# Performance work log

Measured on AMD Instinct MI355X. Metric: run time of the kernel, lower is better.

## Reference

```python
import jax, jax.numpy as jnp
import numpy as np

N_NODES = 10000
N_EDGES = 80000
F_NODE = 16
F_EDGE = 8
BN_EPS = 1e-5


def _nnconv(x, src, dst, edge_attr, w1, b1, w2, b2, w_root, bias, cin, cout):
    # edge MLP -> per-edge weight matrices [E, cin, cout]
    h = jax.nn.relu(edge_attr @ w1 + b1) @ w2 + b2
    w = h.reshape(-1, cin, cout)
    # gather source node features, per-edge matmul
    msg = jnp.einsum('ei,eio->eo', x[src], w)  # [E, cout]
    # scatter-mean into target nodes
    deg = jax.ops.segment_sum(jnp.ones(msg.shape[0], x.dtype), dst, num_segments=N_NODES)
    agg = jax.ops.segment_sum(msg, dst, num_segments=N_NODES) / jnp.clip(deg, 1.0)[:, None]
    return x @ w_root + agg + bias


def _batchnorm(x, gamma, beta):
    m = jnp.mean(x, axis=0)
    v = jnp.mean((x - m) ** 2, axis=0)  # biased var, as torch BN training mode
    return (x - m) * jax.lax.rsqrt(v + BN_EPS) * gamma + beta


def setup_inputs() -> dict:
    key = jax.random.key(0)
    ks = jax.random.split(key, 24)
    s = 0.05
    inp = {
        'x': jax.random.normal(ks[0], (N_NODES, F_NODE), jnp.float32),
        'edge_index': jax.random.randint(ks[1], (2, N_EDGES), 0, N_NODES, jnp.int32),
        'edge_attr': jax.random.normal(ks[2], (N_EDGES, F_EDGE), jnp.float32),
        # conv1 edge MLP: F_EDGE -> 25 -> 32*F_NODE
        'nn1_w1': jax.random.normal(ks[3], (F_EDGE, 25), jnp.float32) * s,
        'nn1_b1': jnp.zeros((25,), jnp.float32),
        'nn1_w2': jax.random.normal(ks[4], (25, 32 * F_NODE), jnp.float32) * s,
        'nn1_b2': jnp.zeros((32 * F_NODE,), jnp.float32),
        'conv1_root': jax.random.normal(ks[5], (F_NODE, 32), jnp.float32) * s,
        'conv1_bias': jnp.zeros((32,), jnp.float32),
        'bn1_gamma': jnp.ones((32,), jnp.float32),
        'bn1_beta': jnp.zeros((32,), jnp.float32),
        # conv2 edge MLP: F_EDGE -> 25 -> 32*64
        'nn2_w1': jax.random.normal(ks[6], (F_EDGE, 25), jnp.float32) * s,
        'nn2_b1': jnp.zeros((25,), jnp.float32),
        'nn2_w2': jax.random.normal(ks[7], (25, 32 * 64), jnp.float32) * s,
        'nn2_b2': jnp.zeros((32 * 64,), jnp.float32),
        'conv2_root': jax.random.normal(ks[8], (32, 64), jnp.float32) * s,
        'conv2_bias': jnp.zeros((64,), jnp.float32),
        'bn2_gamma': jnp.ones((64,), jnp.float32),
        'bn2_beta': jnp.zeros((64,), jnp.float32),
        'fc1_w': jax.random.normal(ks[9], (64, 128), jnp.float32) * s,
        'fc1_b': jnp.zeros((128,), jnp.float32),
        'fc2_w': jax.random.normal(ks[10], (128, 1), jnp.float32) * s,
        'fc2_b': jnp.zeros((1,), jnp.float32),
    }
    return inp


def reference(x, edge_index, edge_attr,
              nn1_w1, nn1_b1, nn1_w2, nn1_b2, conv1_root, conv1_bias, bn1_gamma, bn1_beta,
              nn2_w1, nn2_b1, nn2_w2, nn2_b2, conv2_root, conv2_bias, bn2_gamma, bn2_beta,
              fc1_w, fc1_b, fc2_w, fc2_b):
    src, dst = edge_index[0], edge_index[1]
    h = jax.nn.elu(_nnconv(x, src, dst, edge_attr, nn1_w1, nn1_b1, nn1_w2, nn1_b2,
                           conv1_root, conv1_bias, F_NODE, 32))
    h = jax.nn.elu(_batchnorm(h, bn1_gamma, bn1_beta))
    h = jax.nn.elu(_nnconv(h, src, dst, edge_attr, nn2_w1, nn2_b1, nn2_w2, nn2_b2,
                           conv2_root, conv2_bias, 32, 64))
    h = jax.nn.elu(_batchnorm(h, bn2_gamma, bn2_beta))
    h = jax.nn.elu(h @ fc1_w + fc1_b)
    h = jax.nn.elu(h @ fc2_w + fc2_b)  # [N, 1]
    # single graph: sum over all nodes -> shape [1]
    return jnp.sum(h).reshape(1)
```

## Files before the change

### kernel.cpp

```cpp
#include <hip/hip_runtime.h>
#include <hip/hip_fp16.h>

#define N_NODES 10000
#define N_EDGES 80000
#define FN 16
#define FE 8
#define HID 25
#define C1 32
#define C2 64
#define HROW 28
#define SLOTS 40
#define SC_BLOCKS ((N_EDGES + 255) / 256)
#define NU_BLOCKS 512
#define FC_BLOCKS 640
#define TB1 16
#define TB2 8
#define M1 ((HID + 1) * C1)
#define M2 ((HID + 1) * C2)

typedef _Float16 h16;
typedef _Float16 h16x4 __attribute__((ext_vector_type(4)));

__device__ __forceinline__ float elu_f(float x) { return x > 0.f ? x : (expf(x) - 1.f); }

__device__ __forceinline__ float hdot(const h16* __restrict__ row, const float* Pk) {
    const h16x4* rv = (const h16x4*)row;
    float sx = 0.f, sy = 0.f, sz = 0.f, sw = 0.f;
#pragma unroll
    for (int q = 0; q < 7; q++) {
        h16x4 hv = rv[q];
        sx += (float)hv.x * Pk[4 * q];
        sy += (float)hv.y * Pk[4 * q + 1];
        sz += (float)hv.z * Pk[4 * q + 2];
        sw += (float)hv.w * Pk[4 * q + 3];
    }
    return (sx + sy) + (sz + sw);
}

__device__ __forceinline__ void msg1_edges(const float* Pk, int beg, int end,
                                           const int* __restrict__ ebuf,
                                           const h16* __restrict__ h1r,
                                           float* __restrict__ agg, int lane, int o) {
    int idx = beg;
    for (; idx + 3 < end; idx += 4) {
        int p0 = ebuf[idx], p1 = ebuf[idx + 1], p2 = ebuf[idx + 2], p3 = ebuf[idx + 3];
        float s0 = hdot(h1r + (size_t)(p0 >> 14) * HROW, Pk);
        float s1 = hdot(h1r + (size_t)(p1 >> 14) * HROW, Pk);
        float s2 = hdot(h1r + (size_t)(p2 >> 14) * HROW, Pk);
        float s3 = hdot(h1r + (size_t)(p3 >> 14) * HROW, Pk);
        float va = (lane < 32) ? s0 : s1;
        int da = (lane < 32) ? (p0 & 0x3FFF) : (p1 & 0x3FFF);
        atomicAdd(&agg[da * C1 + o], va);
        float vb = (lane < 32) ? s2 : s3;
        int db = (lane < 32) ? (p2 & 0x3FFF) : (p3 & 0x3FFF);
        atomicAdd(&agg[db * C1 + o], vb);
    }
    for (; idx + 1 < end; idx += 2) {
        int p0 = ebuf[idx], p1 = ebuf[idx + 1];
        float s0 = hdot(h1r + (size_t)(p0 >> 14) * HROW, Pk);
        float s1 = hdot(h1r + (size_t)(p1 >> 14) * HROW, Pk);
        float va = (lane < 32) ? s0 : s1;
        int da = (lane < 32) ? (p0 & 0x3FFF) : (p1 & 0x3FFF);
        atomicAdd(&agg[da * C1 + o], va);
    }
    if (idx < end) {
        int p0 = ebuf[idx];
        float s0 = hdot(h1r + (size_t)(p0 >> 14) * HROW, Pk);
        if (lane < 32) atomicAdd(&agg[(p0 & 0x3FFF) * C1 + o], s0);
    }
}

__device__ __forceinline__ void msg2_edges(const float* Pk, int beg, int end,
                                           const int* __restrict__ ebuf,
                                           const h16* __restrict__ h2r,
                                           float* __restrict__ agg, int lane) {
    int idx = beg;
    for (; idx + 3 < end; idx += 4) {
        int p0 = ebuf[idx], p1 = ebuf[idx + 1], p2 = ebuf[idx + 2], p3 = ebuf[idx + 3];
        float s0 = hdot(h2r + (size_t)(p0 >> 14) * HROW, Pk);
        float s1 = hdot(h2r + (size_t)(p1 >> 14) * HROW, Pk);
        float s2 = hdot(h2r + (size_t)(p2 >> 14) * HROW, Pk);
        float s3 = hdot(h2r + (size_t)(p3 >> 14) * HROW, Pk);
        atomicAdd(&agg[(p0 & 0x3FFF) * C2 + lane], s0);
        atomicAdd(&agg[(p1 & 0x3FFF) * C2 + lane], s1);
        atomicAdd(&agg[(p2 & 0x3FFF) * C2 + lane], s2);
        atomicAdd(&agg[(p3 & 0x3FFF) * C2 + lane], s3);
    }
    for (; idx < end; idx++) {
        int p0 = ebuf[idx];
        float s0 = hdot(h2r + (size_t)(p0 >> 14) * HROW, Pk);
        atomicAdd(&agg[(p0 & 0x3FFF) * C2 + lane], s0);
    }
}

__global__ void k_scatter(const float* __restrict__ ea, const int* __restrict__ ei,
                          const float* __restrict__ w1a, const float* __restrict__ b1a,
                          const float* __restrict__ w1b, const float* __restrict__ b1b,
                          int* __restrict__ cnt_src, int* __restrict__ cnt_dst,
                          int* __restrict__ ebuf, h16* __restrict__ h1r,
                          h16* __restrict__ h2r) {
    int tid = threadIdx.x;
    __shared__ float sw1a[FE * HID], sw1b[FE * HID], sb1a[HID], sb1b[HID];
    for (int i = tid; i < FE * HID; i += 256) { sw1a[i] = w1a[i]; sw1b[i] = w1b[i]; }
    if (tid < HID) { sb1a[tid] = b1a[tid]; sb1b[tid] = b1b[tid]; }
    __syncthreads();
    int e = blockIdx.x * 256 + tid;
    if (e >= N_EDGES) return;
    float a[FE];
#pragma unroll
    for (int i = 0; i < FE; i++) a[i] = ea[e * FE + i];
    int src = ei[e], dst = ei[N_EDGES + e];
    int slot = atomicAdd(&cnt_src[src], 1);
    if (slot < SLOTS) ebuf[src * SLOTS + slot] = (e << 14) | dst;
    atomicAdd(&cnt_dst[dst], 1);
    h16 b1buf[HROW], b2buf[HROW];
#pragma unroll
    for (int k = 0; k < HID; k++) {
        float s1 = sb1a[k], s2 = sb1b[k];
#pragma unroll
        for (int i = 0; i < FE; i++) { s1 += a[i] * sw1a[i * HID + k]; s2 += a[i] * sw1b[i * HID + k]; }
        b1buf[k] = (h16)fmaxf(s1, 0.f);
        b2buf[k] = (h16)fmaxf(s2, 0.f);
    }
    b1buf[25] = (h16)1.f; b1buf[26] = (h16)0.f; b1buf[27] = (h16)0.f;
    b2buf[25] = (h16)1.f; b2buf[26] = (h16)0.f; b2buf[27] = (h16)0.f;
    h16x4* h1p = (h16x4*)(h1r + (size_t)e * HROW);
    h16x4* h2p = (h16x4*)(h2r + (size_t)e * HROW);
#pragma unroll
    for (int q = 0; q < 7; q++) {
        h1p[q] = ((const h16x4*)b1buf)[q];
        h2p[q] = ((const h16x4*)b2buf)[q];
    }
}

__global__ __launch_bounds__(256, 4)
void k_conv1(const float* __restrict__ x, const float* __restrict__ w2,
             const float* __restrict__ b2, const int* __restrict__ cnt_src,
             const int* __restrict__ ebuf, const h16* __restrict__ h1r,
             float* __restrict__ agg) {
    __shared__ h16 Pl[TB1 * M1];
    __shared__ float xs[TB1 * FN];
    int tid = threadIdx.x;
    int n0 = blockIdx.x * TB1;
    for (int t = tid; t < TB1 * FN; t += 256) xs[t] = x[(size_t)n0 * FN + t];
    __syncthreads();
#pragma unroll
    for (int mm = 0; mm < 4; mm++) {
        int m = mm * 256 + tid;
        if (m < M1) {
            int k = m >> 5, o = m & 31;
            float wreg[FN];
            if (k < HID) {
#pragma unroll
                for (int i = 0; i < FN; i++) wreg[i] = w2[(size_t)(k * FN + i) * C1 + o];
            } else {
#pragma unroll
                for (int i = 0; i < FN; i++) wreg[i] = b2[i * C1 + o];
            }
#pragma unroll 2
            for (int n = 0; n < TB1; n++) {
                float s0 = 0.f, s1 = 0.f, s2 = 0.f, s3 = 0.f;
#pragma unroll
                for (int i = 0; i < FN; i += 4) {
                    s0 += xs[n * FN + i]     * wreg[i];
                    s1 += xs[n * FN + i + 1] * wreg[i + 1];
                    s2 += xs[n * FN + i + 2] * wreg[i + 2];
                    s3 += xs[n * FN + i + 3] * wreg[i + 3];
                }
                Pl[n * M1 + m] = (h16)((s0 + s1) + (s2 + s3));
            }
        }
    }
    __syncthreads();
    int lane = tid & 63, wv = tid >> 6, o = lane & 31;
    for (int dn = wv; dn < TB1; dn += 4) {
        int n = n0 + dn;
        float Pk[HROW];
#pragma unroll
        for (int k = 0; k <= HID; k++) Pk[k] = (float)Pl[dn * M1 + k * C1 + o];
        Pk[26] = 0.f; Pk[27] = 0.f;
        int deg = cnt_src[n];
        deg = deg < SLOTS ? deg : SLOTS;
        msg1_edges(Pk, n * SLOTS, n * SLOTS + deg, ebuf, h1r, agg, lane, o);
    }
}

template <int CIN, int COUT>
__global__ void k_node_update(const float* __restrict__ xin, const float* __restrict__ root,
                              const float* __restrict__ bias, const float* __restrict__ agg,
                              const int* __restrict__ degi, float* __restrict__ act,
                              float* __restrict__ s1g, float* __restrict__ s2g,
                              float* zero_out) {
    __shared__ float l1[256], l2[256];
    int tid = threadIdx.x;
    if (zero_out && blockIdx.x == 0 && tid == 0) *zero_out = 0.f;
    int o = tid % COUT;
    float b = bias[o];
    float rcol[CIN];
#pragma unroll
    for (int i = 0; i < CIN; i++) rcol[i] = root[i * COUT + o];
    float acc1 = 0.f, acc2 = 0.f;
    for (int t = blockIdx.x * 256 + tid; t < N_NODES * COUT; t += NU_BLOCKS * 256) {
        int n = t / COUT;
        const float* xr = xin + (size_t)n * CIN;
        float s0 = b, s1 = 0.f, s2 = 0.f, s3 = 0.f;
#pragma unroll
        for (int i = 0; i < CIN; i += 4) {
            s0 += xr[i]     * rcol[i];
            s1 += xr[i + 1] * rcol[i + 1];
            s2 += xr[i + 2] * rcol[i + 2];
            s3 += xr[i + 3] * rcol[i + 3];
        }
        float s = (s0 + s1) + (s2 + s3);
        s += agg[t] / fmaxf((float)degi[n], 1.0f);
        float a = elu_f(s);
        act[t] = a;
        acc1 += a; acc2 += a * a;
    }
    l1[tid] = acc1; l2[tid] = acc2;
    __syncthreads();
    for (int s = 128; s >= COUT; s >>= 1) {
        if (tid < s) { l1[tid] += l1[tid + s]; l2[tid] += l2[tid + s]; }
        __syncthreads();
    }
    if (tid < COUT) { atomicAdd(&s1g[tid], l1[tid]); atomicAdd(&s2g[tid], l2[tid]); }
}

__global__ __launch_bounds__(256, 4)
void k_conv2(const float* __restrict__ a1, const float* __restrict__ s1g,
             const float* __restrict__ s2g, const float* __restrict__ gamma,
             const float* __restrict__ beta, const float* __restrict__ w2,
             const float* __restrict__ b2, const int* __restrict__ cnt_src,
             const int* __restrict__ ebuf, const h16* __restrict__ h2r,
             float* __restrict__ agg, float* __restrict__ h1v) {
    __shared__ h16 Pl[TB2 * M2];
    __shared__ float xs[TB2 * C1];
    int tid = threadIdx.x;
    int n0 = blockIdx.x * TB2;
    for (int t = tid; t < TB2 * C1; t += 256) {
        int o = t & 31;
        float m = s1g[o] * (1.0f / N_NODES);
        float v = s2g[o] * (1.0f / N_NODES) - m * m;
        float sc = rsqrtf(v + 1e-5f) * gamma[o];
        float sh = beta[o] - m * sc;
        float val = elu_f(a1[(size_t)n0 * C1 + t] * sc + sh);
        xs[t] = val;
        h1v[(size_t)n0 * C1 + t] = val;
    }
    __syncthreads();
#pragma unroll
    for (int mm = 0; mm < 7; mm++) {
        int m = mm * 256 + tid;
        if (m < M2) {
            int k = m >> 6, o = m & 63;
            float wreg[C1];
            if (k < HID) {
#pragma unroll
                for (int i = 0; i < C1; i++) wreg[i] = w2[(size_t)(k * C1 + i) * C2 + o];
            } else {
#pragma unroll
                for (int i = 0; i < C1; i++) wreg[i] = b2[i * C2 + o];
            }
#pragma unroll 2
            for (int n = 0; n < TB2; n++) {
                float s0 = 0.f, s1 = 0.f, s2 = 0.f, s3 = 0.f;
#pragma unroll
                for (int i = 0; i < C1; i += 4) {
                    s0 += xs[n * C1 + i]     * wreg[i];
                    s1 += xs[n * C1 + i + 1] * wreg[i + 1];
                    s2 += xs[n * C1 + i + 2] * wreg[i + 2];
                    s3 += xs[n * C1 + i + 3] * wreg[i + 3];
                }
                Pl[n * M2 + m] = (h16)((s0 + s1) + (s2 + s3));
            }
        }
    }
    __syncthreads();
    int lane = tid & 63, wv = tid >> 6;
    for (int dn = wv; dn < TB2; dn += 4) {
        int n = n0 + dn;
        float Pk[HROW];
#pragma unroll
        for (int k = 0; k <= HID; k++) Pk[k] = (float)Pl[dn * M2 + k * C2 + lane];
        Pk[26] = 0.f; Pk[27] = 0.f;
        int deg = cnt_src[n];
        deg = deg < SLOTS ? deg : SLOTS;
        msg2_edges(Pk, n * SLOTS, n * SLOTS + deg, ebuf, h2r, agg, lane);
    }
}

__global__ void k_fc_sum(const float* __restrict__ a2,
                         const float* __restrict__ s1g, const float* __restrict__ s2g,
                         const float* __restrict__ gamma, const float* __restrict__ beta,
                         const float* __restrict__ fc1w, const float* __restrict__ fc1b,
                         const float* __restrict__ fc2w, const float* __restrict__ fc2b,
                         float* __restrict__ out) {
    int tid = threadIdx.x;
    int lane = tid & 63;
    int wave = tid >> 6;
    float m = s1g[lane] * (1.0f / N_NODES);
    float var = s2g[lane] * (1.0f / N_NODES) - m * m;
    float scale = rsqrtf(var + 1e-5f) * gamma[lane];
    float shift = beta[lane] - m * scale;
    float b0 = fc1b[lane], b1 = fc1b[lane + 64];
    float w0 = fc2w[lane], w1 = fc2w[lane + 64];
    float fb = fc2b[0];
    float acc = 0.f;
    for (int n = blockIdx.x * 4 + wave; n < N_NODES; n += FC_BLOCKS * 4) {
        float hval = elu_f(a2[(size_t)n * C2 + lane] * scale + shift);
        float s0 = b0, s1 = b1;
#pragma unroll
        for (int i = 0; i < C2; i++) {
            float hv = __shfl(hval, i);
            s0 += hv * fc1w[i * 128 + lane];
            s1 += hv * fc1w[i * 128 + 64 + lane];
        }
        float v = elu_f(s0) * w0 + elu_f(s1) * w1;
#pragma unroll
        for (int off2 = 32; off2 > 0; off2 >>= 1) v += __shfl_down(v, off2);
        if (lane == 0) acc += elu_f(v + fb);
    }
    __shared__ float lds[4];
    if (lane == 0) lds[wave] = acc;
    __syncthreads();
    if (tid == 0) atomicAdd(out, lds[0] + lds[1] + lds[2] + lds[3]);
}

extern "C" void kernel_launch(void* const* d_in, const int* in_sizes, int n_in,
                              void* d_out, int out_size, void* d_ws, size_t ws_size,
                              hipStream_t stream) {
    const float* x       = (const float*)d_in[0];
    const int*   ei      = (const int*)d_in[1];
    const float* ea      = (const float*)d_in[2];
    const float* nn1_w1  = (const float*)d_in[3];
    const float* nn1_b1  = (const float*)d_in[4];
    const float* nn1_w2  = (const float*)d_in[5];
    const float* nn1_b2  = (const float*)d_in[6];
    const float* c1_root = (const float*)d_in[7];
    const float* c1_bias = (const float*)d_in[8];
    const float* bn1_g   = (const float*)d_in[9];
    const float* bn1_b   = (const float*)d_in[10];
    const float* nn2_w1  = (const float*)d_in[11];
    const float* nn2_b1  = (const float*)d_in[12];
    const float* nn2_w2  = (const float*)d_in[13];
    const float* nn2_b2  = (const float*)d_in[14];
    const float* c2_root = (const float*)d_in[15];
    const float* c2_bias = (const float*)d_in[16];
    const float* bn2_g   = (const float*)d_in[17];
    const float* bn2_b   = (const float*)d_in[18];
    const float* fc1_w   = (const float*)d_in[19];
    const float* fc1_b   = (const float*)d_in[20];
    const float* fc2_w   = (const float*)d_in[21];
    const float* fc2_b   = (const float*)d_in[22];
    float* out = (float*)d_out;

    char* ws = (char*)d_ws;
    size_t off = 0;
    auto alloc = [&](size_t nbytes) -> void* {
        void* q = (void*)(ws + off);
        off += nbytes;
        off = (off + 255) & ~(size_t)255;
        return q;
    };
    int*   cnt_src = (int*)alloc(N_NODES * 4);
    int*   cnt_dst = (int*)alloc(N_NODES * 4);
    float* agg1    = (float*)alloc((size_t)N_NODES * C1 * 4);
    float* agg2    = (float*)alloc((size_t)N_NODES * C2 * 4);
    float* bn1_s1  = (float*)alloc(C1 * 4);
    float* bn1_s2  = (float*)alloc(C1 * 4);
    float* bn2_s1  = (float*)alloc(C2 * 4);
    float* bn2_s2  = (float*)alloc(C2 * 4);
    size_t zero_bytes = off;
    int*   ebuf = (int*)alloc((size_t)N_NODES * SLOTS * 4);
    h16*   h1r  = (h16*)alloc((size_t)N_EDGES * HROW * 2);
    h16*   h2r  = (h16*)alloc((size_t)N_EDGES * HROW * 2);
    float* a1   = (float*)alloc((size_t)N_NODES * C1 * 4);
    float* h1v  = (float*)alloc((size_t)N_NODES * C1 * 4);
    float* a2   = (float*)alloc((size_t)N_NODES * C2 * 4);
    (void)ws_size; (void)in_sizes; (void)n_in; (void)out_size;

    hipMemsetAsync(d_ws, 0, zero_bytes, stream);

    k_scatter<<<SC_BLOCKS, 256, 0, stream>>>(ea, ei, nn1_w1, nn1_b1, nn2_w1, nn2_b1,
                                             cnt_src, cnt_dst, ebuf, h1r, h2r);
    k_conv1<<<N_NODES / TB1, 256, 0, stream>>>(x, nn1_w2, nn1_b2, cnt_src, ebuf, h1r, agg1);
    k_node_update<FN, C1><<<NU_BLOCKS, 256, 0, stream>>>(x, c1_root, c1_bias, agg1,
                                                         cnt_dst, a1, bn1_s1, bn1_s2, nullptr);
    k_conv2<<<N_NODES / TB2, 256, 0, stream>>>(a1, bn1_s1, bn1_s2, bn1_g, bn1_b,
                                               nn2_w2, nn2_b2, cnt_src, ebuf, h2r, agg2, h1v);
    k_node_update<C1, C2><<<NU_BLOCKS, 256, 0, stream>>>(h1v, c2_root, c2_bias, agg2,
                                                         cnt_dst, a2, bn2_s1, bn2_s2, out);
    k_fc_sum<<<FC_BLOCKS, 256, 0, stream>>>(a2, bn2_s1, bn2_s2, bn2_g, bn2_b,
                                            fc1_w, fc1_b, fc2_w, fc2_b, out);
}
```

Before: 254.5 us.

## Use packed fp16 dot products and precompute conv1 node projections in scatter kernel

```diff
diff --git a/kernel.cpp b/kernel.cpp
--- a/kernel.cpp
+++ b/kernel.cpp
@@ -13,41 +13,43 @@
 #define SC_BLOCKS ((N_EDGES + 255) / 256)
 #define NU_BLOCKS 512
 #define FC_BLOCKS 640
-#define TB1 16
+#define TN 25
 #define TB2 8
 #define M1 ((HID + 1) * C1)
 #define M2 ((HID + 1) * C2)
+#define PRE1_BLOCKS (((M1 + 255) / 256) * (N_NODES / TN))
 
 typedef _Float16 h16;
+typedef _Float16 h16x2 __attribute__((ext_vector_type(2)));
 typedef _Float16 h16x4 __attribute__((ext_vector_type(4)));
+typedef _Float16 h16x8 __attribute__((ext_vector_type(8)));
 
 __device__ __forceinline__ float elu_f(float x) { return x > 0.f ? x : (expf(x) - 1.f); }
 
-__device__ __forceinline__ float hdot(const h16* __restrict__ row, const float* Pk) {
-    const h16x4* rv = (const h16x4*)row;
-    float sx = 0.f, sy = 0.f, sz = 0.f, sw = 0.f;
-#pragma unroll
-    for (int q = 0; q < 7; q++) {
-        h16x4 hv = rv[q];
-        sx += (float)hv.x * Pk[4 * q];
-        sy += (float)hv.y * Pk[4 * q + 1];
-        sz += (float)hv.z * Pk[4 * q + 2];
-        sw += (float)hv.w * Pk[4 * q + 3];
-    }
-    return (sx + sy) + (sz + sw);
-}
-
-__device__ __forceinline__ void msg1_edges(const float* Pk, int beg, int end,
+__device__ __forceinline__ float hdot13(const h16* __restrict__ row, const h16x2* Pk2) {
+    const h16x2* rv = (const h16x2*)row;
+    h16x2 a0 = {(h16)0.f, (h16)0.f};
+    h16x2 a1 = a0;
+#pragma unroll
+    for (int q = 0; q < 12; q += 2) {
+        a0 += rv[q] * Pk2[q];
+        a1 += rv[q + 1] * Pk2[q + 1];
+    }
+    a0 += rv[12] * Pk2[12];
+    return (float)a0.x + (float)a0.y + (float)a1.x + (float)a1.y;
+}
+
+__device__ __forceinline__ void msg1_edges(const h16x2* Pk2, int beg, int end,
                                            const int* __restrict__ ebuf,
                                            const h16* __restrict__ h1r,
                                            float* __restrict__ agg, int lane, int o) {
     int idx = beg;
     for (; idx + 3 < end; idx += 4) {
         int p0 = ebuf[idx], p1 = ebuf[idx + 1], p2 = ebuf[idx + 2], p3 = ebuf[idx + 3];
-        float s0 = hdot(h1r + (size_t)(p0 >> 14) * HROW, Pk);
-        float s1 = hdot(h1r + (size_t)(p1 >> 14) * HROW, Pk);
-        float s2 = hdot(h1r + (size_t)(p2 >> 14) * HROW, Pk);
-        float s3 = hdot(h1r + (size_t)(p3 >> 14) * HROW, Pk);
+        float s0 = hdot13(h1r + (size_t)(p0 >> 14) * HROW, Pk2);
+        float s1 = hdot13(h1r + (size_t)(p1 >> 14) * HROW, Pk2);
+        float s2 = hdot13(h1r + (size_t)(p2 >> 14) * HROW, Pk2);
+        float s3 = hdot13(h1r + (size_t)(p3 >> 14) * HROW, Pk2);
         float va = (lane < 32) ? s0 : s1;
         int da = (lane < 32) ? (p0 & 0x3FFF) : (p1 & 0x3FFF);
         atomicAdd(&agg[da * C1 + o], va);
@@ -57,30 +59,30 @@
     }
     for (; idx + 1 < end; idx += 2) {
         int p0 = ebuf[idx], p1 = ebuf[idx + 1];
-        float s0 = hdot(h1r + (size_t)(p0 >> 14) * HROW, Pk);
-        float s1 = hdot(h1r + (size_t)(p1 >> 14) * HROW, Pk);
+        float s0 = hdot13(h1r + (size_t)(p0 >> 14) * HROW, Pk2);
+        float s1 = hdot13(h1r + (size_t)(p1 >> 14) * HROW, Pk2);
         float va = (lane < 32) ? s0 : s1;
         int da = (lane < 32) ? (p0 & 0x3FFF) : (p1 & 0x3FFF);
         atomicAdd(&agg[da * C1 + o], va);
     }
     if (idx < end) {
         int p0 = ebuf[idx];
-        float s0 = hdot(h1r + (size_t)(p0 >> 14) * HROW, Pk);
+        float s0 = hdot13(h1r + (size_t)(p0 >> 14) * HROW, Pk2);
         if (lane < 32) atomicAdd(&agg[(p0 & 0x3FFF) * C1 + o], s0);
     }
 }
 
-__device__ __forceinline__ void msg2_edges(const float* Pk, int beg, int end,
+__device__ __forceinline__ void msg2_edges(const h16x2* Pk2, int beg, int end,
                                            const int* __restrict__ ebuf,
                                            const h16* __restrict__ h2r,
                                            float* __restrict__ agg, int lane) {
     int idx = beg;
     for (; idx + 3 < end; idx += 4) {
         int p0 = ebuf[idx], p1 = ebuf[idx + 1], p2 = ebuf[idx + 2], p3 = ebuf[idx + 3];
-        float s0 = hdot(h2r + (size_t)(p0 >> 14) * HROW, Pk);
-        float s1 = hdot(h2r + (size_t)(p1 >> 14) * HROW, Pk);
-        float s2 = hdot(h2r + (size_t)(p2 >> 14) * HROW, Pk);
-        float s3 = hdot(h2r + (size_t)(p3 >> 14) * HROW, Pk);
+        float s0 = hdot13(h2r + (size_t)(p0 >> 14) * HROW, Pk2);
+        float s1 = hdot13(h2r + (size_t)(p1 >> 14) * HROW, Pk2);
+        float s2 = hdot13(h2r + (size_t)(p2 >> 14) * HROW, Pk2);
+        float s3 = hdot13(h2r + (size_t)(p3 >> 14) * HROW, Pk2);
         atomicAdd(&agg[(p0 & 0x3FFF) * C2 + lane], s0);
         atomicAdd(&agg[(p1 & 0x3FFF) * C2 + lane], s1);
         atomicAdd(&agg[(p2 & 0x3FFF) * C2 + lane], s2);
@@ -88,23 +90,63 @@
     }
     for (; idx < end; idx++) {
         int p0 = ebuf[idx];
-        float s0 = hdot(h2r + (size_t)(p0 >> 14) * HROW, Pk);
+        float s0 = hdot13(h2r + (size_t)(p0 >> 14) * HROW, Pk2);
         atomicAdd(&agg[(p0 & 0x3FFF) * C2 + lane], s0);
     }
 }
 
-__global__ void k_scatter(const float* __restrict__ ea, const int* __restrict__ ei,
-                          const float* __restrict__ w1a, const float* __restrict__ b1a,
-                          const float* __restrict__ w1b, const float* __restrict__ b1b,
-                          int* __restrict__ cnt_src, int* __restrict__ cnt_dst,
-                          int* __restrict__ ebuf, h16* __restrict__ h1r,
-                          h16* __restrict__ h2r) {
+__device__ __forceinline__ void pre1_unit(const float* __restrict__ xin,
+                                          const float* __restrict__ w2,
+                                          const float* __restrict__ b2,
+                                          h16* __restrict__ P, int u, int tid) {
+    constexpr int MB = (M1 + 255) / 256;
+    int mb = u % MB;
+    int n0 = (u / MB) * TN;
+    int m = mb * 256 + tid;
+    if (m >= M1) return;
+    int k = m >> 5, o = m & 31;
+    float wreg[FN];
+    if (k < HID) {
+#pragma unroll
+        for (int i = 0; i < FN; i++) wreg[i] = w2[(size_t)(k * FN + i) * C1 + o];
+    } else {
+#pragma unroll
+        for (int i = 0; i < FN; i++) wreg[i] = b2[i * C1 + o];
+    }
+    int pmo = (k >> 1) * (2 * C1) + o * 2 + (k & 1);
+    for (int n = n0; n < n0 + TN; n++) {
+        const float* xr = xin + (size_t)n * FN;
+        float s0 = 0.f, s1 = 0.f, s2 = 0.f, s3 = 0.f;
+#pragma unroll
+        for (int i = 0; i < FN; i += 4) {
+            s0 += xr[i] * wreg[i];
+            s1 += xr[i + 1] * wreg[i + 1];
+            s2 += xr[i + 2] * wreg[i + 2];
+            s3 += xr[i + 3] * wreg[i + 3];
+        }
+        P[(size_t)n * M1 + pmo] = (h16)((s0 + s1) + (s2 + s3));
+    }
+}
+
+__global__ void k_scatter_pre1(const float* __restrict__ ea, const int* __restrict__ ei,
+                               const float* __restrict__ w1a, const float* __restrict__ b1a,
+                               const float* __restrict__ w1b, const float* __restrict__ b1b,
+                               const float* __restrict__ x, const float* __restrict__ w2a,
+                               const float* __restrict__ b2a,
+                               int* __restrict__ cnt_src, int* __restrict__ cnt_dst,
+                               int* __restrict__ ebuf, h16* __restrict__ h1r,
+                               h16* __restrict__ h2r, h16* __restrict__ P1) {
     int tid = threadIdx.x;
+    int bid = blockIdx.x;
+    if (bid >= SC_BLOCKS) {
+        pre1_unit(x, w2a, b2a, P1, bid - SC_BLOCKS, tid);
+        return;
+    }
     __shared__ float sw1a[FE * HID], sw1b[FE * HID], sb1a[HID], sb1b[HID];
     for (int i = tid; i < FE * HID; i += 256) { sw1a[i] = w1a[i]; sw1b[i] = w1b[i]; }
     if (tid < HID) { sb1a[tid] = b1a[tid]; sb1b[tid] = b1b[tid]; }
     __syncthreads();
-    int e = blockIdx.x * 256 + tid;
+    int e = bid * 256 + tid;
     if (e >= N_EDGES) return;
     float a[FE];
 #pragma unroll
@@ -133,56 +175,20 @@
     }
 }
 
-__global__ __launch_bounds__(256, 4)
-void k_conv1(const float* __restrict__ x, const float* __restrict__ w2,
-             const float* __restrict__ b2, const int* __restrict__ cnt_src,
-             const int* __restrict__ ebuf, const h16* __restrict__ h1r,
-             float* __restrict__ agg) {
-    __shared__ h16 Pl[TB1 * M1];
-    __shared__ float xs[TB1 * FN];
-    int tid = threadIdx.x;
-    int n0 = blockIdx.x * TB1;
-    for (int t = tid; t < TB1 * FN; t += 256) xs[t] = x[(size_t)n0 * FN + t];
-    __syncthreads();
-#pragma unroll
-    for (int mm = 0; mm < 4; mm++) {
-        int m = mm * 256 + tid;
-        if (m < M1) {
-            int k = m >> 5, o = m & 31;
-            float wreg[FN];
-            if (k < HID) {
-#pragma unroll
-                for (int i = 0; i < FN; i++) wreg[i] = w2[(size_t)(k * FN + i) * C1 + o];
-            } else {
-#pragma unroll
-                for (int i = 0; i < FN; i++) wreg[i] = b2[i * C1 + o];
-            }
-#pragma unroll 2
-            for (int n = 0; n < TB1; n++) {
-                float s0 = 0.f, s1 = 0.f, s2 = 0.f, s3 = 0.f;
-#pragma unroll
-                for (int i = 0; i < FN; i += 4) {
-                    s0 += xs[n * FN + i]     * wreg[i];
-                    s1 += xs[n * FN + i + 1] * wreg[i + 1];
-                    s2 += xs[n * FN + i + 2] * wreg[i + 2];
-                    s3 += xs[n * FN + i + 3] * wreg[i + 3];
-                }
-                Pl[n * M1 + m] = (h16)((s0 + s1) + (s2 + s3));
-            }
-        }
-    }
-    __syncthreads();
-    int lane = tid & 63, wv = tid >> 6, o = lane & 31;
-    for (int dn = wv; dn < TB1; dn += 4) {
-        int n = n0 + dn;
-        float Pk[HROW];
-#pragma unroll
-        for (int k = 0; k <= HID; k++) Pk[k] = (float)Pl[dn * M1 + k * C1 + o];
-        Pk[26] = 0.f; Pk[27] = 0.f;
-        int deg = cnt_src[n];
-        deg = deg < SLOTS ? deg : SLOTS;
-        msg1_edges(Pk, n * SLOTS, n * SLOTS + deg, ebuf, h1r, agg, lane, o);
-    }
+__global__ void k_conv1(const h16x2* __restrict__ P1p, const int* __restrict__ cnt_src,
+                        const int* __restrict__ ebuf, const h16* __restrict__ h1r,
+                        float* __restrict__ agg) {
+    int lane = threadIdx.x & 63;
+    int o = lane & 31;
+    int n = __builtin_amdgcn_readfirstlane(blockIdx.x * 4 + (threadIdx.x >> 6));
+    if (n >= N_NODES) return;
+    h16x2 Pk2[13];
+    const h16x2* Pr = P1p + (size_t)n * (M1 / 2) + o;
+#pragma unroll
+    for (int kk = 0; kk < 13; kk++) Pk2[kk] = Pr[kk * C1];
+    int deg = cnt_src[n];
+    deg = deg < SLOTS ? deg : SLOTS;
+    msg1_edges(Pk2, n * SLOTS, n * SLOTS + deg, ebuf, h1r, agg, lane, o);
 }
 
 template <int CIN, int COUT>
@@ -233,59 +239,70 @@
              const float* __restrict__ b2, const int* __restrict__ cnt_src,
              const int* __restrict__ ebuf, const h16* __restrict__ h2r,
              float* __restrict__ agg, float* __restrict__ h1v) {
-    __shared__ h16 Pl[TB2 * M2];
-    __shared__ float xs[TB2 * C1];
+    __shared__ h16 Pl_h[TB2 * M2];
+    __shared__ h16 xs_h[C1 * TB2];
     int tid = threadIdx.x;
     int n0 = blockIdx.x * TB2;
-    for (int t = tid; t < TB2 * C1; t += 256) {
-        int o = t & 31;
+    {
+        int n = tid >> 5, o = tid & 31;
         float m = s1g[o] * (1.0f / N_NODES);
         float v = s2g[o] * (1.0f / N_NODES) - m * m;
         float sc = rsqrtf(v + 1e-5f) * gamma[o];
         float sh = beta[o] - m * sc;
-        float val = elu_f(a1[(size_t)n0 * C1 + t] * sc + sh);
-        xs[t] = val;
-        h1v[(size_t)n0 * C1 + t] = val;
+        float val = elu_f(a1[(size_t)n0 * C1 + tid] * sc + sh);
+        xs_h[o * TB2 + n] = (h16)val;
+        h1v[(size_t)n0 * C1 + tid] = val;
     }
     __syncthreads();
+    const h16x8* xsv = (const h16x8*)xs_h;
 #pragma unroll
     for (int mm = 0; mm < 7; mm++) {
         int m = mm * 256 + tid;
         if (m < M2) {
             int k = m >> 6, o = m & 63;
-            float wreg[C1];
+            h16x2 wh[C1];
             if (k < HID) {
 #pragma unroll
-                for (int i = 0; i < C1; i++) wreg[i] = w2[(size_t)(k * C1 + i) * C2 + o];
+                for (int i = 0; i < C1; i++) {
+                    h16 w = (h16)w2[(size_t)(k * C1 + i) * C2 + o];
+                    wh[i] = (h16x2){w, w};
+                }
             } else {
 #pragma unroll
-                for (int i = 0; i < C1; i++) wreg[i] = b2[i * C2 + o];
+                for (int i = 0; i < C1; i++) {
+                    h16 w = (h16)b2[i * C2 + o];
+                    wh[i] = (h16x2){w, w};
+                }
             }
-#pragma unroll 2
-            for (int n = 0; n < TB2; n++) {
-                float s0 = 0.f, s1 = 0.f, s2 = 0.f, s3 = 0.f;
-#pragma unroll
-                for (int i = 0; i < C1; i += 4) {
-                    s0 += xs[n * C1 + i]     * wreg[i];
-                    s1 += xs[n * C1 + i + 1] * wreg[i + 1];
-                    s2 += xs[n * C1 + i + 2] * wreg[i + 2];
-                    s3 += xs[n * C1 + i + 3] * wreg[i + 3];
-                }
-                Pl[n * M2 + m] = (h16)((s0 + s1) + (s2 + s3));
+            h16x2 acc0 = {(h16)0.f, (h16)0.f};
+            h16x2 acc1 = acc0, acc2 = acc0, acc3 = acc0;
+#pragma unroll
+            for (int i = 0; i < C1; i++) {
+                h16x8 xv = xsv[i];
+                acc0 += __builtin_shufflevector(xv, xv, 0, 1) * wh[i];
+                acc1 += __builtin_shufflevector(xv, xv, 2, 3) * wh[i];
+                acc2 += __builtin_shufflevector(xv, xv, 4, 5) * wh[i];
+                acc3 += __builtin_shufflevector(xv, xv, 6, 7) * wh[i];
             }
+            int pmo = (k >> 1) * (2 * C2) + o * 2 + (k & 1);
+            h16* Plr = Pl_h + pmo;
+            Plr[0 * M2] = acc0.x; Plr[1 * M2] = acc0.y;
+            Plr[2 * M2] = acc1.x; Plr[3 * M2] = acc1.y;
+            Plr[4 * M2] = acc2.x; Plr[5 * M2] = acc2.y;
+            Plr[6 * M2] = acc3.x; Plr[7 * M2] = acc3.y;
         }
     }
     __syncthreads();
+    const h16x2* Plp = (const h16x2*)Pl_h;
     int lane = tid & 63, wv = tid >> 6;
     for (int dn = wv; dn < TB2; dn += 4) {
         int n = n0 + dn;
-        float Pk[HROW];
-#pragma unroll
-        for (int k = 0; k <= HID; k++) Pk[k] = (float)Pl[dn * M2 + k * C2 + lane];
-        Pk[26] = 0.f; Pk[27] = 0.f;
+        h16x2 Pk2[13];
+#pragma unroll
+        for (int kk = 0; kk < 13; kk++) Pk2[kk] = Plp[dn * (M2 / 2) + kk * C2 + lane];
         int deg = cnt_src[n];
         deg = deg < SLOTS ? deg : SLOTS;
-        msg2_edges(Pk, n * SLOTS, n * SLOTS + deg, ebuf, h2r, agg, lane);
+        msg2_edges(Pk2, n * SLOTS, n * SLOTS + deg, ebuf, h2r, agg, lane);
     }
 }
 
@@ -374,6 +391,7 @@
     int*   ebuf = (int*)alloc((size_t)N_NODES * SLOTS * 4);
     h16*   h1r  = (h16*)alloc((size_t)N_EDGES * HROW * 2);
     h16*   h2r  = (h16*)alloc((size_t)N_EDGES * HROW * 2);
+    h16*   P1   = (h16*)alloc((size_t)N_NODES * M1 * 2);
     float* a1   = (float*)alloc((size_t)N_NODES * C1 * 4);
     float* h1v  = (float*)alloc((size_t)N_NODES * C1 * 4);
     float* a2   = (float*)alloc((size_t)N_NODES * C2 * 4);
@@ -381,9 +399,10 @@
 
     hipMemsetAsync(d_ws, 0, zero_bytes, stream);
 
-    k_scatter<<<SC_BLOCKS, 256, 0, stream>>>(ea, ei, nn1_w1, nn1_b1, nn2_w1, nn2_b1,
-                                             cnt_src, cnt_dst, ebuf, h1r, h2r);
-    k_conv1<<<N_NODES / TB1, 256, 0, stream>>>(x, nn1_w2, nn1_b2, cnt_src, ebuf, h1r, agg1);
+    k_scatter_pre1<<<SC_BLOCKS + PRE1_BLOCKS, 256, 0, stream>>>(
+        ea, ei, nn1_w1, nn1_b1, nn2_w1, nn2_b1, x, nn1_w2, nn1_b2,
+        cnt_src, cnt_dst, ebuf, h1r, h2r, P1);
+    k_conv1<<<(N_NODES + 3) / 4, 256, 0, stream>>>((const h16x2*)P1, cnt_src, ebuf, h1r, agg1);
     k_node_update<FN, C1><<<NU_BLOCKS, 256, 0, stream>>>(x, c1_root, c1_bias, agg1,
                                                          cnt_dst, a1, bn1_s1, bn1_s2, nullptr);
     k_conv2<<<N_NODES / TB2, 256, 0, stream>>>(a1, bn1_s1, bn1_s2, bn1_g, bn1_b,
```

Result: faster. 228.3 us (-10.3%).
